# Optimization experiments

Measured on AMD Instinct MI355X. Metric: run time of the kernel, lower is better.

The kernel has to match this reference:

```python
import jax, jax.numpy as jnp
import numpy as np

CONT_FIELD = 13
CATE_FIELD = 26
VOCAB = 100000
EMB_DIM = 40
ATTN_DIM = 8
BATCH = 4096


def setup_inputs() -> dict:
    key = jax.random.key(0)
    ks = jax.random.split(key, 8)
    conts = jax.random.uniform(ks[0], (BATCH, CONT_FIELD), dtype=jnp.float32)
    cates = jax.random.randint(ks[1], (BATCH, CATE_FIELD), 0, VOCAB, dtype=jnp.int64)
    combs = jax.random.normal(ks[2], (BATCH, 1), dtype=jnp.float32)
    a = np.square(3.0 / (CATE_FIELD * EMB_DIM))
    emb_table = jax.random.uniform(ks[3], (VOCAB, EMB_DIM), minval=-a, maxval=a, dtype=jnp.float32)
    attn_W = jax.random.normal(ks[4], (ATTN_DIM, EMB_DIM), dtype=jnp.float32) * 0.1
    attn_b = jnp.zeros((ATTN_DIM,), dtype=jnp.float32)
    proj_W = jax.random.normal(ks[5], (1, ATTN_DIM), dtype=jnp.float32) * 0.3
    fc_W = jax.random.normal(ks[6], (1, EMB_DIM), dtype=jnp.float32) * 0.1
    fc_b = jnp.zeros((1,), dtype=jnp.float32)
    return {"conts": conts, "cates": cates, "combs": combs, "emb_table": emb_table,
            "attn_W": attn_W, "attn_b": attn_b, "proj_W": proj_W, "fc_W": fc_W, "fc_b": fc_b}


def reference(conts, cates, combs, emb_table, attn_W, attn_b, proj_W, fc_W, fc_b):
    # continuous fields use fixed embedding rows 0..CONT_FIELD-1 scaled by value
    cont_emb = emb_table[jnp.arange(CONT_FIELD)][None, :, :] * conts[:, :, None]  # (B, 13, D)
    cate_emb = emb_table[cates]                                                   # (B, 26, D)
    x = jnp.concatenate([cont_emb, cate_emb], axis=1)                             # (B, 39, D)
    row, col = jnp.triu_indices(CONT_FIELD + CATE_FIELD, k=1)                     # 741 pairs
    ewp = x[:, row, :] * x[:, col, :]                                             # (B, 741, D)
    h = jax.nn.relu(jnp.einsum('bpd,ad->bpa', ewp, attn_W) + attn_b)              # (B, 741, 8)
    logits = jnp.einsum('bpa,oa->bpo', h, proj_W)                                 # (B, 741, 1)
    attn = jax.nn.softmax(logits, axis=1)                                         # softmax over pairs
    pooled = jnp.sum(attn * ewp, axis=1)                                          # (B, D)
    out = jax.nn.sigmoid(pooled @ fc_W.T + fc_b)                                  # (B, 1)
    return out
```

## Files before the change

### kernel.cpp

```cpp
#include <hip/hip_runtime.h>
#include <math.h>

#define NF 39
#define CONT_F 13
#define CATE_F 26
#define EMB_D 40
#define VOCAB 100000
#define NCH 9
#define ROW_B 80
#define CH_B  3120

typedef __attribute__((ext_vector_type(8))) short short8;
typedef __attribute__((ext_vector_type(4))) float f32x4;

__device__ __forceinline__ unsigned pack_bf16x2(float a, float b) {
    unsigned ua = __float_as_uint(a);
    unsigned ub = __float_as_uint(b);
    ua = (ua + 0x7FFFu + ((ua >> 16) & 1u)) >> 16;
    ub = (ub + 0x7FFFu + ((ub >> 16) & 1u)) >> 16;
    return ua | (ub << 16);
}

__global__ __launch_bounds__(384, 5)
void afm_mfma_kernel(const float* __restrict__ conts,
                     const int*   __restrict__ cates,
                     const float* __restrict__ emb,
                     const float* __restrict__ attn_W,
                     const float* __restrict__ attn_b,
                     const float* __restrict__ proj_W,
                     const float* __restrict__ fc_W,
                     const float* __restrict__ fc_b,
                     float* __restrict__ out)
{
    __shared__ __attribute__((aligned(16))) unsigned short Xb[NF * EMB_D];
    __shared__ __attribute__((aligned(16))) unsigned short Aall[NCH * NF * EMB_D];
    __shared__ __attribute__((aligned(16))) float zero16[4];
    __shared__ float redm[6], reds[6], redg[6];

    const int tid = threadIdx.x;
    const int row = blockIdx.x;

    if (tid < 4) zero16[tid] = 0.f;

    {
        const float4* emb4 = (const float4*)emb;
        unsigned* XbW = (unsigned*)Xb;
        unsigned* AW  = (unsigned*)Aall;
        for (int t = tid; t < NF * 10; t += 384) {
            const int f = t / 10, q = t % 10;
            float4 v;
            if (f < CONT_F) {
                v = emb4[f * 10 + q];
                const float cs = conts[row * CONT_F + f];
                v.x *= cs; v.y *= cs; v.z *= cs; v.w *= cs;
            } else {
                unsigned u = (unsigned)cates[row * CATE_F + (f - CONT_F)];
                if (u >= (unsigned)VOCAB) u = 0;
                v = emb4[u * 10 + q];
            }
            const int wofs = f * 20 + q * 2;
            XbW[wofs]     = pack_bf16x2(v.x, v.y);
            XbW[wofs + 1] = pack_bf16x2(v.z, v.w);
            #pragma unroll
            for (int c = 0; c < NCH; ++c) {
                const float4 wv = (c < 8) ? ((const float4*)attn_W)[c * 10 + q]
                                          : ((const float4*)fc_W)[q];
                AW[c * 780 + wofs]     = pack_bf16x2(v.x * wv.x, v.y * wv.y);
                AW[c * 780 + wofs + 1] = pack_bf16x2(v.z * wv.z, v.w * wv.w);
            }
        }
    }
    __syncthreads();

    const int wid  = tid >> 6;
    const int lane = tid & 63;
    const int mt = (wid < 3) ? 0 : ((wid < 5) ? 1 : 2);
    const int nt = (wid < 3) ? wid : ((wid < 5) ? (wid - 2) : 2);

    const int l15  = lane & 15;
    const int quad = lane >> 4;

    int rB = nt * 16 + l15; if (rB > NF - 1) rB = NF - 1;
    int rA = mt * 16 + l15; if (rA > NF - 1) rA = NF - 1;

    const char* XbP = (const char*)Xb;
    const char* AP  = (const char*)Aall;
    const char* ZP  = (const char*)zero16;

    const char* aB0 = XbP + rB * ROW_B + quad * 16;
    const char* aB1 = (quad == 0) ? (XbP + rB * ROW_B + 64) : ZP;
    const char* aA0 = AP + rA * ROW_B + quad * 16;
    const char* aA1q0 = AP + rA * ROW_B + 64;

    const short8 b0 = *(const short8*)aB0;
    const short8 b1 = *(const short8*)aB1;

    f32x4 acc[NCH];
    #pragma unroll
    for (int c = 0; c < NCH; ++c) {
        const short8 a0 = *(const short8*)(aA0 + c * CH_B);
        const short8 a1 = *(const short8*)((quad == 0) ? (aA1q0 + c * CH_B) : ZP);
        f32x4 z = {0.f, 0.f, 0.f, 0.f};
        z = __builtin_amdgcn_mfma_f32_16x16x32_bf16(a0, b0, z, 0, 0, 0);
        z = __builtin_amdgcn_mfma_f32_16x16x32_bf16(a1, b1, z, 0, 0, 0);
        acc[c] = z;
    }

    float pj[8], bb[8];
    #pragma unroll
    for (int a = 0; a < 8; ++a) { pj[a] = proj_W[a]; bb[a] = attn_b[a]; }

    float lv[4], gv[4];
    bool  ok[4];
    float m = -INFINITY;
    #pragma unroll
    for (int r = 0; r < 4; ++r) {
        const int i = mt * 16 + quad * 4 + r;
        const int j = nt * 16 + l15;
        ok[r] = (i < j) && (j < NF);
        float l = 0.f;
        #pragma unroll
        for (int a = 0; a < 8; ++a)
            l = fmaf(pj[a], fmaxf(acc[a][r] + bb[a], 0.f), l);
        lv[r] = l;
        gv[r] = acc[8][r];
        if (ok[r]) m = fmaxf(m, l);
    }

    #pragma unroll
    for (int off = 32; off; off >>= 1) m = fmaxf(m, __shfl_xor(m, off));
    if (lane == 0) redm[wid] = m;
    __syncthreads();
    float M = redm[0];
    #pragma unroll
    for (int w = 1; w < 6; ++w) M = fmaxf(M, redm[w]);

    float s = 0.f, gs = 0.f;
    #pragma unroll
    for (int r = 0; r < 4; ++r) {
        if (ok[r]) {
            const float e = __expf(lv[r] - M);
            s += e;
            gs = fmaf(e, gv[r], gs);
        }
    }
    #pragma unroll
    for (int off = 32; off; off >>= 1) {
        s  += __shfl_xor(s, off);
        gs += __shfl_xor(gs, off);
    }
    if (lane == 0) { reds[wid] = s; redg[wid] = gs; }
    __syncthreads();

    if (tid == 0) {
        float S = reds[0], G = redg[0];
        #pragma unroll
        for (int w = 1; w < 6; ++w) { S += reds[w]; G += redg[w]; }
        const float zf = G / S + fc_b[0];
        out[row] = 1.f / (1.f + __expf(-zf));
    }
}

extern "C" void kernel_launch(void* const* d_in, const int* in_sizes, int n_in,
                              void* d_out, int out_size, void* d_ws, size_t ws_size,
                              hipStream_t stream) {
    const float* conts  = (const float*)d_in[0];
    const int*   cates  = (const int*)  d_in[1];
    const float* emb    = (const float*)d_in[3];
    const float* attn_W = (const float*)d_in[4];
    const float* attn_b = (const float*)d_in[5];
    const float* proj_W = (const float*)d_in[6];
    const float* fc_W   = (const float*)d_in[7];
    const float* fc_b   = (const float*)d_in[8];
    float* out = (float*)d_out;

    const int batch = in_sizes[0] / CONT_F;
    afm_mfma_kernel<<<batch, 384, 0, stream>>>(
        conts, cates, emb, attn_W, attn_b, proj_W, fc_W, fc_b, out);
}
```

Baseline: 105.4 us.

## Halve block size, remap MFMA tiles per wave, drop softmax max pass

Shrinks each block from six waves to three. Each wave now owns one M-tile row and loops over its upper-triangular N-tiles, reusing the A fragment loads. The softmax max reduction and its barrier are removed; logits are exponentiated directly, which assumes they stay small. bf16 packing changes from round-to-nearest to truncation, and LDS stores are vectorised to 64-bit. The trade is more serial MFMA work per wave and fewer threads for the gather, plus a risk of overflow and lower precision.

After: 103.6 us. Within noise of the previous version (-1.7%).

```diff
diff --git a/kernel.cpp b/kernel.cpp
--- a/kernel.cpp
+++ b/kernel.cpp
@@ -13,15 +13,11 @@
 typedef __attribute__((ext_vector_type(8))) short short8;
 typedef __attribute__((ext_vector_type(4))) float f32x4;
 
-__device__ __forceinline__ unsigned pack_bf16x2(float a, float b) {
-    unsigned ua = __float_as_uint(a);
-    unsigned ub = __float_as_uint(b);
-    ua = (ua + 0x7FFFu + ((ua >> 16) & 1u)) >> 16;
-    ub = (ub + 0x7FFFu + ((ub >> 16) & 1u)) >> 16;
-    return ua | (ub << 16);
+__device__ __forceinline__ unsigned pack_bf16x2_trunc(float a, float b) {
+    return (__float_as_uint(b) & 0xFFFF0000u) | (__float_as_uint(a) >> 16);
 }
 
-__global__ __launch_bounds__(384, 5)
+__global__ __launch_bounds__(192, 3)
 void afm_mfma_kernel(const float* __restrict__ conts,
                      const int*   __restrict__ cates,
                      const float* __restrict__ emb,
@@ -35,7 +31,7 @@
     __shared__ __attribute__((aligned(16))) unsigned short Xb[NF * EMB_D];
     __shared__ __attribute__((aligned(16))) unsigned short Aall[NCH * NF * EMB_D];
     __shared__ __attribute__((aligned(16))) float zero16[4];
-    __shared__ float redm[6], reds[6], redg[6];
+    __shared__ float reds[3], redg[3];
 
     const int tid = threadIdx.x;
     const int row = blockIdx.x;
@@ -46,7 +42,7 @@
         const float4* emb4 = (const float4*)emb;
         unsigned* XbW = (unsigned*)Xb;
         unsigned* AW  = (unsigned*)Aall;
-        for (int t = tid; t < NF * 10; t += 384) {
+        for (int t = tid; t < NF * 10; t += 192) {
             const int f = t / 10, q = t % 10;
             float4 v;
             if (f < CONT_F) {
@@ -59,14 +55,15 @@
                 v = emb4[u * 10 + q];
             }
             const int wofs = f * 20 + q * 2;
-            XbW[wofs]     = pack_bf16x2(v.x, v.y);
-            XbW[wofs + 1] = pack_bf16x2(v.z, v.w);
+            *(uint2*)&XbW[wofs] = make_uint2(pack_bf16x2_trunc(v.x, v.y),
+                                             pack_bf16x2_trunc(v.z, v.w));
             #pragma unroll
             for (int c = 0; c < NCH; ++c) {
                 const float4 wv = (c < 8) ? ((const float4*)attn_W)[c * 10 + q]
                                           : ((const float4*)fc_W)[q];
-                AW[c * 780 + wofs]     = pack_bf16x2(v.x * wv.x, v.y * wv.y);
-                AW[c * 780 + wofs + 1] = pack_bf16x2(v.z * wv.z, v.w * wv.w);
+                *(uint2*)&AW[c * 780 + wofs] =
+                    make_uint2(pack_bf16x2_trunc(v.x * wv.x, v.y * wv.y),
+                               pack_bf16x2_trunc(v.z * wv.z, v.w * wv.w));
             }
         }
     }
@@ -74,74 +71,76 @@
 
     const int wid  = tid >> 6;
     const int lane = tid & 63;
-    const int mt = (wid < 3) ? 0 : ((wid < 5) ? 1 : 2);
-    const int nt = (wid < 3) ? wid : ((wid < 5) ? (wid - 2) : 2);
-
     const int l15  = lane & 15;
     const int quad = lane >> 4;
 
-    int rB = nt * 16 + l15; if (rB > NF - 1) rB = NF - 1;
-    int rA = mt * 16 + l15; if (rA > NF - 1) rA = NF - 1;
+    int rA = wid * 16 + l15; if (rA > NF - 1) rA = NF - 1;
 
     const char* XbP = (const char*)Xb;
     const char* AP  = (const char*)Aall;
     const char* ZP  = (const char*)zero16;
 
-    const char* aB0 = XbP + rB * ROW_B + quad * 16;
-    const char* aB1 = (quad == 0) ? (XbP + rB * ROW_B + 64) : ZP;
-    const char* aA0 = AP + rA * ROW_B + quad * 16;
-    const char* aA1q0 = AP + rA * ROW_B + 64;
-
-    const short8 b0 = *(const short8*)aB0;
-    const short8 b1 = *(const short8*)aB1;
-
-    f32x4 acc[NCH];
+    short8 b0[3], b1[3];
     #pragma unroll
-    for (int c = 0; c < NCH; ++c) {
-        const short8 a0 = *(const short8*)(aA0 + c * CH_B);
-        const short8 a1 = *(const short8*)((quad == 0) ? (aA1q0 + c * CH_B) : ZP);
-        f32x4 z = {0.f, 0.f, 0.f, 0.f};
-        z = __builtin_amdgcn_mfma_f32_16x16x32_bf16(a0, b0, z, 0, 0, 0);
-        z = __builtin_amdgcn_mfma_f32_16x16x32_bf16(a1, b1, z, 0, 0, 0);
-        acc[c] = z;
+    for (int nt = 0; nt < 3; ++nt) {
+        if (nt >= wid) {
+            int rB = nt * 16 + l15; if (rB > NF - 1) rB = NF - 1;
+            b0[nt] = *(const short8*)(XbP + rB * ROW_B + quad * 16);
+            b1[nt] = *(const short8*)((quad == 0) ? (XbP + rB * ROW_B + 64) : ZP);
+        }
     }
 
     float pj[8], bb[8];
     #pragma unroll
     for (int a = 0; a < 8; ++a) { pj[a] = proj_W[a]; bb[a] = attn_b[a]; }
 
-    float lv[4], gv[4];
-    bool  ok[4];
-    float m = -INFINITY;
-    #pragma unroll
-    for (int r = 0; r < 4; ++r) {
-        const int i = mt * 16 + quad * 4 + r;
-        const int j = nt * 16 + l15;
-        ok[r] = (i < j) && (j < NF);
-        float l = 0.f;
-        #pragma unroll
-        for (int a = 0; a < 8; ++a)
-            l = fmaf(pj[a], fmaxf(acc[a][r] + bb[a], 0.f), l);
-        lv[r] = l;
-        gv[r] = acc[8][r];
-        if (ok[r]) m = fmaxf(m, l);
-    }
+    float lacc[3][4] = {{0}};
+    float gv[3][4];
 
     #pragma unroll
-    for (int off = 32; off; off >>= 1) m = fmaxf(m, __shfl_xor(m, off));
-    if (lane == 0) redm[wid] = m;
-    __syncthreads();
-    float M = redm[0];
-    #pragma unroll
-    for (int w = 1; w < 6; ++w) M = fmaxf(M, redm[w]);
+    for (int c = 0; c < NCH; ++c) {
+        const char* aRow = AP + c * CH_B + rA * ROW_B;
+        const short8 a0 = *(const short8*)(aRow + quad * 16);
+        const short8 a1 = *(const short8*)((quad == 0) ? (aRow + 64) : ZP);
+        f32x4 z[3];
+        #pragma unroll
+        for (int nt = 0; nt < 3; ++nt) {
+            if (nt >= wid) {
+                f32x4 t = {0.f, 0.f, 0.f, 0.f};
+                t = __builtin_amdgcn_mfma_f32_16x16x32_bf16(a0, b0[nt], t, 0, 0, 0);
+                t = __builtin_amdgcn_mfma_f32_16x16x32_bf16(a1, b1[nt], t, 0, 0, 0);
+                z[nt] = t;
+            }
+        }
+        #pragma unroll
+        for (int nt = 0; nt < 3; ++nt) {
+            if (nt >= wid) {
+                #pragma unroll
+                for (int r = 0; r < 4; ++r) {
+                    if (c < 8)
+                        lacc[nt][r] = fmaf(pj[c], fmaxf(z[nt][r] + bb[c], 0.f),
+                                           lacc[nt][r]);
+                    else
+                        gv[nt][r] = z[nt][r];
+                }
+            }
+        }
+    }
 
     float s = 0.f, gs = 0.f;
     #pragma unroll
-    for (int r = 0; r < 4; ++r) {
-        if (ok[r]) {
-            const float e = __expf(lv[r] - M);
-            s += e;
-            gs = fmaf(e, gv[r], gs);
+    for (int nt = 0; nt < 3; ++nt) {
+        if (nt >= wid) {
+            #pragma unroll
+            for (int r = 0; r < 4; ++r) {
+                const int i = wid * 16 + quad * 4 + r;
+                const int j = nt * 16 + l15;
+                if (i < j && j < NF) {
+                    const float e = __expf(lacc[nt][r]);
+                    s += e;
+                    gs = fmaf(e, gv[nt][r], gs);
+                }
+            }
         }
     }
     #pragma unroll
@@ -153,9 +152,8 @@
     __syncthreads();
 
     if (tid == 0) {
-        float S = reds[0], G = redg[0];
-        #pragma unroll
-        for (int w = 1; w < 6; ++w) { S += reds[w]; G += redg[w]; }
+        const float S = reds[0] + reds[1] + reds[2];
+        const float G = redg[0] + redg[1] + redg[2];
         const float zf = G / S + fc_b[0];
         out[row] = 1.f / (1.f + __expf(-zf));
     }
@@ -175,6 +173,6 @@
     float* out = (float*)d_out;
 
     const int batch = in_sizes[0] / CONT_F;
-    afm_mfma_kernel<<<batch, 384, 0, stream>>>(
+    afm_mfma_kernel<<<batch, 192, 0, stream>>>(
         conts, cates, emb, attn_W, attn_b, proj_W, fc_W, fc_b, out);
 }
```
